# Kernel optimization log

Hardware: AMD Instinct MI355X
Metric: run time of the kernel (lower is better)

Reference implementation:

```python
import jax, jax.numpy as jnp
import numpy as np

WINDOW_SIZE = 2
CART_PIXEL_WIDTH = 640
CART_RESOLUTION = 0.2592
# even width -> (w/2 - 0.5) * res
CART_MIN_RANGE = (CART_PIXEL_WIDTH / 2 - 0.5) * CART_RESOLUTION


def setup_inputs() -> dict:
    key = jax.random.key(0)
    k1, k2, k3 = jax.random.split(key, 3)
    B, W, N = 64, WINDOW_SIZE, 100000
    keypoint_coords = jax.random.uniform(k1, (B * W, N, 2), dtype=jnp.float32) * CART_PIXEL_WIDTH
    tgt_coords = jax.random.uniform(k2, (B, N, 2), dtype=jnp.float32) * CART_PIXEL_WIDTH
    weights = jax.random.uniform(k3, (B, 1, N), dtype=jnp.float32) + 1e-3
    return {"keypoint_coords": keypoint_coords, "tgt_coords": tgt_coords, "weights": weights}


def _convert_to_radar_frame(p):
    # p: [B, N, 2] pixel coords -> radar-frame metric coords
    # R = [[0, -res], [res, 0]]; t = [cmin, -cmin]
    x = -CART_RESOLUTION * p[..., 1] + CART_MIN_RANGE
    y = CART_RESOLUTION * p[..., 0] - CART_MIN_RANGE
    return jnp.stack([x, y], axis=-1)  # [B, N, 2]


def _svd_forward(keypoint_coords, tgt_coords, weights):
    src = keypoint_coords[::WINDOW_SIZE]                # [B, N, 2]
    src = _convert_to_radar_frame(src)
    tgt = _convert_to_radar_frame(tgt_coords)
    # pad 2D -> 3D with zeros, then transpose to [B, 3, N]
    src = jnp.pad(src, ((0, 0), (0, 0), (0, 1))).transpose(0, 2, 1)
    tgt = jnp.pad(tgt, ((0, 0), (0, 0), (0, 1))).transpose(0, 2, 1)

    w = jnp.sum(weights, axis=2, keepdims=True)         # [B, 1, 1]
    src_centroid = jnp.sum(src * weights, axis=2, keepdims=True) / w  # [B, 3, 1]
    tgt_centroid = jnp.sum(tgt * weights, axis=2, keepdims=True) / w
    src_c = src - src_centroid
    tgt_c = tgt - tgt_centroid
    # weighted cross-covariance: [B, 3, 3]
    Wc = jnp.einsum('bin,bjn->bij', tgt_c * weights, src_c) / w

    U, _, Vh = jnp.linalg.svd(Wc)                       # square -> full == reduced
    det_UV = jnp.linalg.det(U) * jnp.linalg.det(Vh)     # det(V) == det(Vh) for 3x3? no: det(Vh)=det(V^T)=det(V)
    # R = U @ diag(1, 1, det) @ V^T ; scale last column of U by det
    s = jnp.stack([jnp.ones_like(det_UV), jnp.ones_like(det_UV), det_UV], axis=-1)  # [B, 3]
    R_tgt_src = jnp.einsum('bik,bk,bkj->bij', U, s, Vh)

    t_tgt_src_insrc = src_centroid - jnp.einsum('bki,bkj->bij', R_tgt_src, tgt_centroid)
    t_src_tgt_intgt = -jnp.einsum('bik,bkj->bij', R_tgt_src, t_tgt_src_insrc)
    return R_tgt_src.transpose(0, 2, 1), t_src_tgt_intgt


def reference(keypoint_coords, tgt_coords, weights):
    return _svd_forward(keypoint_coords, tgt_coords, weights)
```

## Files before the change

### kernel.cpp

```cpp
#include <hip/hip_runtime.h>

#define RES  0.2592
#define MINR 82.8144

__global__ __launch_bounds__(256) void svd_reduce(
    const float4* __restrict__ kp,
    const float4* __restrict__ tg,
    const float4* __restrict__ wq4,
    const float2* __restrict__ wt2,
    double* __restrict__ ws,
    int npairs, int bpb)
{
    const int batch  = blockIdx.y;
    const int nquads = npairs >> 1;
    const float4* __restrict__ src = kp  + (size_t)(2 * batch) * npairs;
    const float4* __restrict__ tgt = tg  + (size_t)batch * npairs;
    const float4* __restrict__ wq  = wq4 + (size_t)batch * nquads;

    double aW = 0, aPx = 0, aPy = 0, aQx = 0, aQy = 0;
    double aXX = 0, aXY = 0, aYX = 0, aYY = 0;

    #define POINT(wf, sxf, syf, txf, tyf) do {                 \
        double w  = (double)(wf);                              \
        double sx = (double)(sxf), sy = (double)(syf);         \
        double tx = (double)(txf), ty = (double)(tyf);         \
        double wtx = w * tx, wty = w * ty;                     \
        aW  += w;                                              \
        aPx += w * sx;   aPy += w * sy;                        \
        aQx += wtx;      aQy += wty;                           \
        aXX += wtx * sx; aXY += wtx * sy;                      \
        aYX += wty * sx; aYY += wty * sy;                      \
    } while (0)

    for (int i = blockIdx.x * 256 + threadIdx.x; i < nquads; i += bpb * 256) {
        float4 s0 = src[2 * i], s1 = src[2 * i + 1];
        float4 t0 = tgt[2 * i], t1 = tgt[2 * i + 1];
        float4 w4 = wq[i];
        POINT(w4.x, s0.x, s0.y, t0.x, t0.y);
        POINT(w4.y, s0.z, s0.w, t0.z, t0.w);
        POINT(w4.z, s1.x, s1.y, t1.x, t1.y);
        POINT(w4.w, s1.z, s1.w, t1.z, t1.w);
    }
    if ((npairs & 1) && blockIdx.x == 0 && threadIdx.x == 0) {
        int i = npairs - 1;
        float4 s4 = src[i], t4 = tgt[i];
        float2 w2 = wt2[(size_t)batch * npairs + i];
        POINT(w2.x, s4.x, s4.y, t4.x, t4.y);
        POINT(w2.y, s4.z, s4.w, t4.z, t4.w);
    }
    #undef POINT

    double acc[9] = {aW, aPx, aPy, aQx, aQy, aXX, aXY, aYX, aYY};

    #pragma unroll
    for (int k = 0; k < 9; k++) {
        #pragma unroll
        for (int off = 32; off > 0; off >>= 1)
            acc[k] += __shfl_down(acc[k], off, 64);
    }

    __shared__ double sred[4][9];
    const int lane = threadIdx.x & 63;
    const int wid  = threadIdx.x >> 6;
    if (lane == 0) {
        #pragma unroll
        for (int k = 0; k < 9; k++) sred[wid][k] = acc[k];
    }
    __syncthreads();
    if (threadIdx.x < 9) {
        double v = sred[0][threadIdx.x] + sred[1][threadIdx.x] +
                   sred[2][threadIdx.x] + sred[3][threadIdx.x];
        ws[((size_t)batch * bpb + blockIdx.x) * 9 + threadIdx.x] = v;
    }
}

__global__ void svd_finalize(const double* __restrict__ ws,
                             float* __restrict__ out, int B, int bpb)
{
    int b = blockIdx.x * blockDim.x + threadIdx.x;
    if (b >= B) return;

    double m[9] = {0, 0, 0, 0, 0, 0, 0, 0, 0};
    const double* p = ws + (size_t)b * bpb * 9;
    for (int j = 0; j < bpb; ++j) {
        #pragma unroll
        for (int k = 0; k < 9; ++k) m[k] += p[j * 9 + k];
    }

    double W  = m[0];
    double Px = m[1], Py = m[2], Qx = m[3], Qy = m[4];
    double Rxx = m[5], Rxy = m[6], Ryx = m[7], Ryy = m[8];

    const double MR = MINR * RES, RR = RES * RES;
    double MW = MINR * W;
    double Sx = MW - RES * Py;
    double Sy = RES * Px - MW;
    double Tx = MW - RES * Qy;
    double Ty = RES * Qx - MW;
    double Mxx = MINR * MW - MR * (Py + Qy) + RR * Ryy;
    double Mxy = MR * Px - MINR * MW + MR * Qy - RR * Ryx;
    double Myx = MR * Qx + MR * Py - MINR * MW - RR * Rxy;
    double Myy = RR * Rxx - MR * (Px + Qx) + MINR * MW;

    double invW = 1.0 / W;
    double a  = (Mxx - Tx * Sx * invW) * invW;
    double bb = (Mxy - Tx * Sy * invW) * invW;
    double c  = (Myx - Ty * Sx * invW) * invW;
    double d  = (Myy - Ty * Sy * invW) * invW;

    double h1 = sqrt((a + d) * (a + d) + (bb - c) * (bb - c));
    double h2 = sqrt((a - d) * (a - d) + (bb + c) * (bb + c));

    double q00, q01, q10, q11, sgn;
    if (h1 >= h2) {
        double inv = 1.0 / h1;
        q00 = (a + d) * inv;  q01 = (bb - c) * inv;
        q10 = (c - bb) * inv; q11 = (a + d) * inv;
        sgn = 1.0;
    } else {
        double inv = 1.0 / h2;
        q00 = (a - d) * inv;  q01 = (bb + c) * inv;
        q10 = (bb + c) * inv; q11 = (d - a) * inv;
        sgn = -1.0;
    }

    double sx = Sx * invW, sy = Sy * invW;
    double tx = Tx * invW, ty = Ty * invW;

    double t1x = sx - (q00 * tx + q10 * ty);
    double t1y = sy - (q01 * tx + q11 * ty);
    double ox = -(q00 * t1x + q01 * t1y);
    double oy = -(q10 * t1x + q11 * t1y);

    float* R = out + (size_t)b * 9;
    R[0] = (float)q00; R[1] = (float)q10; R[2] = 0.0f;
    R[3] = (float)q01; R[4] = (float)q11; R[5] = 0.0f;
    R[6] = 0.0f;       R[7] = 0.0f;       R[8] = (float)sgn;

    float* T = out + (size_t)B * 9 + (size_t)b * 3;
    T[0] = (float)ox; T[1] = (float)oy; T[2] = 0.0f;
}

extern "C" void kernel_launch(void* const* d_in, const int* in_sizes, int n_in,
                              void* d_out, int out_size, void* d_ws, size_t ws_size,
                              hipStream_t stream) {
    const float* kp = (const float*)d_in[0];
    const float* tg = (const float*)d_in[1];
    const float* wt = (const float*)d_in[2];
    float* out = (float*)d_out;

    const int B = out_size / 12;
    const int N = in_sizes[2] / B;
    const int npairs = N / 2;
    const int BPB = 32;

    dim3 grid(BPB, B);
    svd_reduce<<<grid, 256, 0, stream>>>(
        (const float4*)kp, (const float4*)tg,
        (const float4*)wt, (const float2*)wt,
        (double*)d_ws, npairs, BPB);

    svd_finalize<<<(B + 63) / 64, 64, 0, stream>>>((const double*)d_ws, out, B, BPB);
}
```

Measured before the change: 208.8 us.

## Process point pairs per thread and parallelize finalize across a wavefront per batch

The main reduction loop now handles one pair of points per iteration (float4 src/tgt plus a float2 weight) instead of four points via a float4 weight load, which drops the odd-tail special case. The partial-sum workspace is transposed to component-major order so the finalize kernel can use one 64-lane wavefront per batch, reading partials in a coalesced way and reducing them with shuffles instead of one thread looping serially. This aims to shorten the serial finalize tail. The cost is smaller loads and less work per thread in the main loop, plus more finalize blocks.

```diff
diff --git a/kernel.cpp b/kernel.cpp
--- a/kernel.cpp
+++ b/kernel.cpp
@@ -6,16 +6,14 @@
 __global__ __launch_bounds__(256) void svd_reduce(
     const float4* __restrict__ kp,
     const float4* __restrict__ tg,
-    const float4* __restrict__ wq4,
-    const float2* __restrict__ wt2,
+    const float2* __restrict__ wt,
     double* __restrict__ ws,
     int npairs, int bpb)
 {
-    const int batch  = blockIdx.y;
-    const int nquads = npairs >> 1;
-    const float4* __restrict__ src = kp  + (size_t)(2 * batch) * npairs;
-    const float4* __restrict__ tgt = tg  + (size_t)batch * npairs;
-    const float4* __restrict__ wq  = wq4 + (size_t)batch * nquads;
+    const int batch = blockIdx.y;
+    const float4* __restrict__ src = kp + (size_t)(2 * batch) * npairs;
+    const float4* __restrict__ tgt = tg + (size_t)batch * npairs;
+    const float2* __restrict__ wp  = wt + (size_t)batch * npairs;
 
     double aW = 0, aPx = 0, aPy = 0, aQx = 0, aQy = 0;
     double aXX = 0, aXY = 0, aYX = 0, aYY = 0;
@@ -32,19 +30,10 @@
         aYX += wty * sx; aYY += wty * sy;                      \
     } while (0)
 
-    for (int i = blockIdx.x * 256 + threadIdx.x; i < nquads; i += bpb * 256) {
-        float4 s0 = src[2 * i], s1 = src[2 * i + 1];
-        float4 t0 = tgt[2 * i], t1 = tgt[2 * i + 1];
-        float4 w4 = wq[i];
-        POINT(w4.x, s0.x, s0.y, t0.x, t0.y);
-        POINT(w4.y, s0.z, s0.w, t0.z, t0.w);
-        POINT(w4.z, s1.x, s1.y, t1.x, t1.y);
-        POINT(w4.w, s1.z, s1.w, t1.z, t1.w);
-    }
-    if ((npairs & 1) && blockIdx.x == 0 && threadIdx.x == 0) {
-        int i = npairs - 1;
-        float4 s4 = src[i], t4 = tgt[i];
-        float2 w2 = wt2[(size_t)batch * npairs + i];
+    for (int i = blockIdx.x * 256 + threadIdx.x; i < npairs; i += bpb * 256) {
+        float4 s4 = src[i];
+        float4 t4 = tgt[i];
+        float2 w2 = wp[i];
         POINT(w2.x, s4.x, s4.y, t4.x, t4.y);
         POINT(w2.y, s4.z, s4.w, t4.z, t4.w);
     }
@@ -70,22 +59,26 @@
     if (threadIdx.x < 9) {
         double v = sred[0][threadIdx.x] + sred[1][threadIdx.x] +
                    sred[2][threadIdx.x] + sred[3][threadIdx.x];
-        ws[((size_t)batch * bpb + blockIdx.x) * 9 + threadIdx.x] = v;
+        ws[((size_t)batch * 9 + threadIdx.x) * bpb + blockIdx.x] = v;
     }
 }
 
-__global__ void svd_finalize(const double* __restrict__ ws,
-                             float* __restrict__ out, int B, int bpb)
+__global__ __launch_bounds__(64) void svd_finalize(
+    const double* __restrict__ ws, float* __restrict__ out, int B, int bpb)
 {
-    int b = blockIdx.x * blockDim.x + threadIdx.x;
-    if (b >= B) return;
+    const int b    = blockIdx.x;
+    const int lane = threadIdx.x;
 
-    double m[9] = {0, 0, 0, 0, 0, 0, 0, 0, 0};
-    const double* p = ws + (size_t)b * bpb * 9;
-    for (int j = 0; j < bpb; ++j) {
+    double m[9];
+    #pragma unroll
+    for (int k = 0; k < 9; k++) {
+        double v = (lane < bpb) ? ws[((size_t)b * 9 + k) * bpb + lane] : 0.0;
         #pragma unroll
-        for (int k = 0; k < 9; ++k) m[k] += p[j * 9 + k];
+        for (int off = 32; off > 0; off >>= 1)
+            v += __shfl_down(v, off, 64);
+        m[k] = v;
     }
+    if (lane != 0) return;
 
     double W  = m[0];
     double Px = m[1], Py = m[2], Qx = m[3], Qy = m[4];
@@ -156,9 +149,8 @@
 
     dim3 grid(BPB, B);
     svd_reduce<<<grid, 256, 0, stream>>>(
-        (const float4*)kp, (const float4*)tg,
-        (const float4*)wt, (const float2*)wt,
+        (const float4*)kp, (const float4*)tg, (const float2*)wt,
         (double*)d_ws, npairs, BPB);
 
-    svd_finalize<<<(B + 63) / 64, 64, 0, stream>>>((const double*)d_ws, out, B, BPB);
+    svd_finalize<<<B, 64, 0, stream>>>((const double*)d_ws, out, B, BPB);
 }
```

New measurement: 196.5 us. -5.9%, faster.
